# Performance work log

Measured on AMD Instinct MI355X. Metric: run time of the kernel, lower is better.

Reference implementation:

```python
import jax, jax.numpy as jnp
import numpy as np

# ---- constants derived from init kwargs (sr == down_sr => resample is identity) ----
SR = 16000
DOWN_SR = 16000
FRAME_TIME = 0.01
FMIN, FMAX = 75.0, 600.0
K = 15
TH_SIL, TH_VOI = 0.03, 0.45
C_OCT, C_JUMP, C_VUV = 0.01, 0.35, 0.14
MED = 5
STRIDES = int(DOWN_SR * FRAME_TIME)          # 160
TMAX = int(DOWN_SR // FMIN)                  # 213
TMIN = int(DOWN_SR // FMAX)                  # 26
W = int(2 ** np.ceil(np.log2(TMAX))) + 1     # 257
FLOOR = -100000.0


def setup_inputs() -> dict:
    key = jax.random.key(0)
    inputs = jax.random.normal(key, (16, 960000), dtype=jnp.float32) * 0.3
    return {"inputs": inputs}


def _nacf_forward(inputs):
    # window / normalized-autocorrelation window (buffers)
    window = 0.5 * (1.0 - jnp.cos(2.0 * jnp.pi * jnp.arange(W, dtype=jnp.float32) / W))  # periodic hann
    r = jnp.fft.rfft(window, 2 * W)
    ws = jnp.fft.irfft(r * jnp.conj(r), 2 * W)[:W]
    nacw = ws / ws[0]

    x = inputs  # resample(sr=16k -> 16k) is identity
    T = x.shape[-1]
    S = T // STRIDES + 1  # number of frames after right-pad by W
    xpad = jnp.pad(x, [(0, 0), (0, W)])
    fidx = jnp.arange(S)[:, None] * STRIDES + jnp.arange(W)[None, :]
    frames = xpad[:, fidx]                                      # [B, S, W]
    frames = (frames - frames.mean(-1, keepdims=True)) * window

    global_peak = jnp.abs(inputs).max(-1)                       # [B]
    local_peak = jnp.abs(frames).max(-1)                        # [B, S]
    intensity = jnp.where(local_peak > global_peak[:, None], 1.0,
                          local_peak / global_peak[:, None])

    # FFT-based autocorrelation, normalized
    fft = jnp.fft.rfft(frames, 2 * W, axis=-1)
    acf = jnp.fft.irfft(fft * jnp.conj(fft), 2 * W, axis=-1)[..., :W]
    nacf = acf / (acf[..., :1] * nacw)
    nacf = nacf[..., :TMAX + 1]                                 # [B, S, TMAX+1]

    d = jnp.diff(nacf, axis=-1)
    localmax = (d[..., :-1] >= 0) & (d[..., 1:] <= 0)
    flag = localmax & (nacf[..., 1:-1] > 0.5 * TH_VOI)

    n_, c_, p_ = nacf[..., 2:], nacf[..., 1:-1], nacf[..., :-2]
    dr = 0.5 * (n_ - p_) / (2.0 * c_ - n_ - p_)                 # parabolic interp
    a = jnp.arange(TMAX - 1, dtype=jnp.float32)
    freqs = DOWN_SR / (1.0 + jnp.maximum(dr + a, 0.0))          # [B, S, TMAX-1]

    logits = nacf[..., 1:TMAX]
    logits = jnp.where(logits <= 1.0, logits, 1.0 / logits)
    logits = logits - C_OCT * jnp.log2(FMIN / freqs)
    logits = jnp.where(flag, logits, FLOOR)

    logits, indices = jax.lax.top_k(logits, K)                  # [B, S, K]
    freqs = jnp.take_along_axis(freqs, indices, axis=-1)

    logits_uv = 2.0 - intensity / (TH_SIL / (1.0 + TH_VOI))
    logits_uv = TH_VOI + jnp.maximum(logits_uv, 0.0)            # [B, S]

    voiced = (logits > FLOOR) & (freqs < FMAX)                  # [B, S, K]
    delta = jnp.where(~voiced, logits_uv[..., None],
                      logits - C_OCT * jnp.log2(FMAX / freqs))

    vi = voiced[:, :-1, :, None]
    vj = voiced[:, 1:, None, :]
    trans = C_JUMP * jnp.abs(jnp.log2(freqs[:, :-1, :, None] / freqs[:, 1:, None, :]))
    trans = jnp.where(~vi & ~vj, 0.0, trans)
    trans = jnp.where(vi != vj, C_VUV, trans)                   # [B, S-1, K, K]

    # ---- Viterbi forward (scan over time) ----
    delta_t = jnp.moveaxis(delta, 1, 0)                         # [S, B, K]
    trans_t = jnp.moveaxis(trans, 1, 0)                         # [S-1, B, K, K]

    def fstep(value, xs):
        tr, dl = xs
        scores = value[..., :, None] - tr + dl[..., None, :]    # [B, K(prev), K(cur)]
        return scores.max(-2), scores.argmax(-2)

    value, ptrs = jax.lax.scan(fstep, delta_t[0], (trans_t, delta_t[1:]))

    # ---- backtrack (reverse scan) ----
    last = jnp.argmax(value, axis=-1)                           # [B]

    def bstep(s, ptr_t):
        s_new = jnp.take_along_axis(ptr_t, s[..., None], axis=-1)[..., 0]
        return s_new, s_new

    _, states_rev = jax.lax.scan(bstep, last, ptrs, reverse=True)  # [S-1, B]
    states = jnp.concatenate([jnp.moveaxis(states_rev, 0, 1), last[:, None]], axis=-1)  # [B, S]

    f_sel = jnp.take_along_axis(freqs, states[..., None], axis=-1)[..., 0]
    v_sel = jnp.take_along_axis(voiced, states[..., None], axis=-1)[..., 0]
    f0 = jnp.where(v_sel, f_sel, 0.0)                           # [B, S]

    wpad = MED // 2
    fpad = jnp.pad(f0, [(0, 0), (wpad, wpad)], mode='edge')
    widx = jnp.arange(f0.shape[-1])[:, None] + jnp.arange(MED)[None, :]
    f0 = jnp.median(fpad[:, widx], axis=-1)
    return f0


def reference(inputs):
    return _nacf_forward(inputs)
```

## Files before the change

### kernel.cpp

```cpp
#include <hip/hip_runtime.h>

#define NB 16
#define NT 960000
#define NS 6001
#define TOPK 15
#define NSTEPS 6000
#define CHUNK 100
#define NCHUNK 60
#define FLOORV -100000.0f

typedef __attribute__((ext_vector_type(8))) short short8;
typedef __attribute__((ext_vector_type(4))) float f32x4;
typedef __attribute__((ext_vector_type(2))) float f32x2;
typedef __attribute__((ext_vector_type(4))) unsigned int u32x4;

constexpr size_t OFF_NACW  = 0;
constexpr size_t OFF_WIN   = 256;
constexpr size_t OFF_GPEAK = 520;
constexpr size_t OFF_FREQ  = 576;
constexpr size_t PERFR     = (size_t)NB * NS * 16;
constexpr size_t OFF_LFV   = OFF_FREQ + PERFR;
constexpr size_t OFF_DELTA = OFF_LFV + PERFR;
constexpr size_t OFF_UNUSED= OFF_DELTA + PERFR;
constexpr size_t OFF_P     = OFF_UNUSED + PERFR;
constexpr size_t OFF_VENT  = OFF_P + (size_t)NB * NCHUNK * 256;
constexpr size_t OFF_VFIN  = OFF_VENT + (size_t)NB * (NCHUNK + 1) * 16;
constexpr size_t OFF_F0    = OFF_VFIN + 256;
constexpr size_t OFF_BS    = OFF_F0 + 96032;
constexpr size_t OFF_PTR   = OFF_BS + 2048;
constexpr size_t OFF_BMAP  = OFF_PTR + (size_t)NB * NSTEPS * 4;

__device__ __forceinline__ unsigned ordf(float f) {
  unsigned u = __float_as_uint(f);
  return (u & 0x80000000u) ? ~u : (u | 0x80000000u);
}

__device__ __forceinline__ float tr_of(float sa, float sb) {
  int xs = __float_as_int(sa) ^ __float_as_int(sb);
  float t = 0.35f * fabsf(sa - sb);
  t = (__float_as_int(sa) < 0) ? 0.f : t;
  return (xs < 0) ? 0.14f : t;
}

__global__ __launch_bounds__(256) void k_setup(float* __restrict__ ws) {
  __shared__ float win[257];
  __shared__ float w0sh;
  const int tid = threadIdx.x;
  for (int n = tid; n < 257; n += 256) {
    float w = 0.5f * (1.0f - cosf((6.2831855f * (float)n) / 257.0f));
    win[n] = w;
    ws[OFF_WIN + n] = w;
  }
  __syncthreads();
  float s = 0.f;
  if (tid < 216) {
    for (int n = 0; n + tid < 257; ++n) s += win[n] * win[n + tid];
  }
  if (tid == 0) w0sh = s;
  __syncthreads();
  if (tid < 216) ws[OFF_NACW + tid] = w0sh / s;
  if (tid < NB) ws[OFF_GPEAK + tid] = 0.0f;
}

__global__ __launch_bounds__(256) void k_gpeak(const float* __restrict__ x, float* __restrict__ ws) {
  const int b = blockIdx.y;
  const float4* xb = (const float4*)(x + (size_t)b * NT);
  const int n4 = NT / 4;
  float m = 0.f;
  for (int i = blockIdx.x * blockDim.x + threadIdx.x; i < n4; i += gridDim.x * blockDim.x) {
    float4 v = xb[i];
    m = fmaxf(m, fmaxf(fmaxf(fabsf(v.x), fabsf(v.y)), fmaxf(fabsf(v.z), fabsf(v.w))));
  }
  for (int off = 32; off; off >>= 1) m = fmaxf(m, __shfl_down(m, off));
  __shared__ float sm[4];
  if ((threadIdx.x & 63) == 0) sm[threadIdx.x >> 6] = m;
  __syncthreads();
  if (threadIdx.x == 0) {
    m = fmaxf(fmaxf(sm[0], sm[1]), fmaxf(sm[2], sm[3]));
    atomicMax((unsigned*)(ws + OFF_GPEAK) + b, __float_as_uint(m));
  }
}

__device__ __forceinline__ unsigned bf16rne(float f) {
  unsigned u = __float_as_uint(f);
  return (u + 0x7FFFu + ((u >> 16) & 1u)) >> 16;
}

__device__ __forceinline__ short8 bfrag(const char* p, int sh) {
  unsigned w0 = *(const unsigned*)(p);
  unsigned w1 = *(const unsigned*)(p + 4);
  unsigned w2 = *(const unsigned*)(p + 8);
  unsigned w3 = *(const unsigned*)(p + 12);
  unsigned w4 = *(const unsigned*)(p + 16);
  u32x4 o;
  o[0] = __builtin_amdgcn_alignbit(w1, w0, sh);
  o[1] = __builtin_amdgcn_alignbit(w2, w1, sh);
  o[2] = __builtin_amdgcn_alignbit(w3, w2, sh);
  o[3] = __builtin_amdgcn_alignbit(w4, w3, sh);
  return __builtin_bit_cast(short8, o);
}

__global__ __launch_bounds__(256, 4) void k_frames(const float* __restrict__ x, float* __restrict__ ws) {
  const int wv = threadIdx.x >> 6;
  const int g  = threadIdx.x & 63;
  const int s  = blockIdx.x * 4 + wv;
  const int b  = blockIdx.y;
  __shared__ __align__(16) float LA[4][1680];
  if (s >= NS) return;
  float* L = LA[wv];
  char* Lb = (char*)L;
  const size_t xb = (size_t)b * NT;
  const int c0 = 40 * s;

  float4 xv = make_float4(0.f, 0.f, 0.f, 0.f);
  if (c0 + g < NT / 4) xv = ((const float4*)(x + xb))[c0 + g];
  float x256 = 0.f;
  if (g == 0) {
    int i256 = 160 * s + 256;
    if (i256 < NT) x256 = x[xb + i256];
  }

  float ps = ((xv.x + xv.y) + (xv.z + xv.w)) + x256;
#pragma unroll
  for (int off = 32; off; off >>= 1) ps += __shfl_xor(ps, off);
  const float mean = ps / 257.0f;

  float4 w4 = ((const float4*)(ws + OFF_WIN))[g];
  float4 f4;
  f4.x = (xv.x - mean) * w4.x;
  f4.y = (xv.y - mean) * w4.y;
  f4.z = (xv.z - mean) * w4.z;
  f4.w = (xv.w - mean) * w4.w;
  float fr256 = 0.f;
  if (g == 0) fr256 = (x256 - mean) * ws[OFF_WIN + 256];
  float apk = fmaxf(fmaxf(fabsf(f4.x), fabsf(f4.y)), fmaxf(fabsf(f4.z), fabsf(f4.w)));
  if (g == 0) apk = fmaxf(apk, fabsf(fr256));
#pragma unroll
  for (int off = 32; off; off >>= 1) apk = fmaxf(apk, __shfl_xor(apk, off));

  {
    unsigned hx = bf16rne(f4.x), hy = bf16rne(f4.y), hz = bf16rne(f4.z), hw = bf16rne(f4.w);
    float lx = f4.x - __uint_as_float(hx << 16);
    float ly = f4.y - __uint_as_float(hy << 16);
    float lz = f4.z - __uint_as_float(hz << 16);
    float lw = f4.w - __uint_as_float(hw << 16);
    unsigned ph0 = hx | (hy << 16), ph1 = hz | (hw << 16);
    unsigned pl0 = bf16rne(lx) | (bf16rne(ly) << 16);
    unsigned pl1 = bf16rne(lz) | (bf16rne(lw) << 16);
    if (g < 8) { L[g] = 0.f; L[288 + g] = 0.f; }
    f32x2 vh = {__uint_as_float(ph0), __uint_as_float(ph1)};
    f32x2 vl = {__uint_as_float(pl0), __uint_as_float(pl1)};
    *(f32x2*)&L[8 + 2 * g] = vh;
    *(f32x2*)&L[288 + 8 + 2 * g] = vl;
    if (g < 76) {
      f32x2 z = {0.f, 0.f};
      *(f32x2*)&L[136 + 2 * g] = z;
      *(f32x2*)&L[288 + 136 + 2 * g] = z;
    }
    if (g == 0) {
      unsigned h2 = bf16rne(fr256);
      float l2 = fr256 - __uint_as_float(h2 << 16);
      ((unsigned short*)Lb)[272] = (unsigned short)h2;
      ((unsigned short*)(Lb + 1152))[272] = (unsigned short)bf16rne(l2);
    }
  }
  __builtin_amdgcn_wave_barrier();

  const int bcol = g & 15, h = g >> 4;
  const int sh = 16 * (bcol & 1);
  const int hi4 = ((bcol & 3) >= 2) ? 4 : 0;
  const int Ab0 = 16 * h + 32 * bcol;
  const int Bb0 = 16 * h + ((2 * bcol) & ~7) + hi4;
  const char* Hb = Lb;
  const char* Ob = Lb + 1152;
  f32x4 acc = {0.f, 0.f, 0.f, 0.f};
#pragma unroll
  for (int kk = 0; kk < 10; ++kk) {
    short8 ah = __builtin_bit_cast(short8, *(const u32x4*)(Hb + Ab0 + 64 * kk));
    short8 al = __builtin_bit_cast(short8, *(const u32x4*)(Ob + Ab0 + 64 * kk));
    short8 bh = bfrag(Hb + Bb0 + 64 * kk, sh);
    short8 bl = bfrag(Ob + Bb0 + 64 * kk, sh);
    acc = __builtin_amdgcn_mfma_f32_16x16x32_bf16(ah, bh, acc, 0, 0, 0);
    acc = __builtin_amdgcn_mfma_f32_16x16x32_bf16(ah, bl, acc, 0, 0, 0);
    acc = __builtin_amdgcn_mfma_f32_16x16x32_bf16(al, bh, acc, 0, 0, 0);
  }
  __builtin_amdgcn_wave_barrier();
#pragma unroll
  for (int r = 0; r < 4; ++r) {
    int arow = 4 * h + r;
    int tau = 16 * arow - bcol;
    if (arow == 0 ? (bcol == 0) : (tau <= 215)) L[576 + (arow ? tau : 0)] = acc[r];
  }
  __builtin_amdgcn_wave_barrier();

  const float inv0 = 1.0f / L[576];
  bool  flv[4] = {false, false, false, false};
  float lgv[4];
  if (g < 53) {
    f32x4 A4 = *(const f32x4*)&L[576 + 4 * g];
    f32x2 A2 = *(const f32x2*)&L[580 + 4 * g];
    f32x4 I4 = *(const f32x4*)(ws + OFF_NACW + 4 * g);
    f32x2 I2 = *(const f32x2*)(ws + OFF_NACW + 4 * g + 4);
    float nn[6];
    nn[0] = A4[0] * inv0 * I4[0];
    nn[1] = A4[1] * inv0 * I4[1];
    nn[2] = A4[2] * inv0 * I4[2];
    nn[3] = A4[3] * inv0 * I4[3];
    nn[4] = A2.x * inv0 * I2.x;
    nn[5] = A2.y * inv0 * I2.y;
    float fqv[4];
#pragma unroll
    for (int a = 0; a < 4; ++a) {
      float pm = nn[a], cm = nn[a + 1], nm = nn[a + 2];
      bool flag = (cm - pm >= 0.f) && (nm - cm <= 0.f) && (cm > 0.225f);
      float dr = (0.5f * (nm - pm)) / ((2.0f * cm - nm) - pm);
      float tq = dr + (float)(4 * g + a);
      tq = (tq > 0.f) ? tq : 0.f;
      float fq = 16000.0f / (1.0f + tq);
      float l1p = __log2f(1.0f + tq);
      float lg = cm;
      if (lg > 1.0f) lg = __builtin_amdgcn_rcpf(lg);
      lg = lg - 0.01f * (l1p - 7.736965594166206f);
      flv[a] = flag;
      fqv[a] = fq;
      lgv[a] = flag ? lg : FLOORV;
    }
    f32x4 fo = {fqv[0], fqv[1], fqv[2], fqv[3]};
    f32x4 lo_ = {lgv[0], lgv[1], lgv[2], lgv[3]};
    *(f32x4*)&L[800 + 4 * g] = fo;
    *(f32x4*)&L[1016 + 4 * g] = lo_;
  }

  unsigned long long bb0b = __ballot(flv[0]);
  unsigned long long bb1 = __ballot(flv[1]);
  unsigned long long bb2 = __ballot(flv[2]);
  unsigned long long bb3 = __ballot(flv[3]);
  const int nv = __popcll(bb0b) + __popcll(bb1) + __popcll(bb2) + __popcll(bb3);
  int* sel = (int*)&L[1656];
  if (nv > 0) {
    unsigned long long below = (1ull << g) - 1ull;
    int base = __popcll(bb0b & below) + __popcll(bb1 & below) +
               __popcll(bb2 & below) + __popcll(bb3 & below);
    if (nv <= TOPK) {
      if (g < 53) {
        int cnt = base;
#pragma unroll
        for (int a = 0; a < 4; ++a) {
          int c = 4 * g + a;
          if (flv[a]) {
            sel[cnt] = c;
            ++cnt;
          } else {
            int ur = c - cnt;
            if (ur < TOPK - nv) sel[nv + ur] = c;
          }
        }
      }
    } else {
      unsigned long long* CK = (unsigned long long*)&L[1232];
      if (g < 53) {
        int cnt = base;
#pragma unroll
        for (int a = 0; a < 4; ++a) {
          if (flv[a]) {
            CK[cnt] = (((unsigned long long)ordf(lgv[a])) << 32)
                    | (unsigned long long)(0xFFFFFFFFu - (unsigned)(4 * g + a));
            ++cnt;
          }
        }
      }
      __builtin_amdgcn_wave_barrier();
      for (int l = g; l < nv; l += 64) {
        unsigned long long kl = CK[l];
        int rank = 0;
        for (int m = 0; m < nv; ++m) rank += (CK[m] > kl) ? 1 : 0;
        if (rank < TOPK) sel[rank] = (int)(0xFFFFFFFFu - (unsigned)(kl & 0xFFFFFFFFull));
      }
    }
  }
  __builtin_amdgcn_wave_barrier();

  if (g < 16) {
    size_t fi = ((size_t)b * NS + s) * 16 + g;
    if (g == TOPK) {
      ws[OFF_FREQ + fi] = 0.f;
      ws[OFF_LFV + fi] = -1.0f;
      ws[OFF_DELTA + fi] = 0.f;
    } else {
      int c = (nv == 0) ? g : sel[g];
      float fq = L[800 + c];
      float lg = L[1016 + c];
      int voi = (lg > FLOORV) && (fq < 600.0f);
      float gp = ws[OFF_GPEAK + b];
      float inten = (apk > gp) ? 1.0f : apk * __builtin_amdgcn_rcpf(gp);
      float luv = 0.45f + fmaxf(2.0f - inten * 48.333333333333336f, 0.f);
      float l2 = __log2f(fq);
      float dlt = voi ? (lg - 0.01f * (9.228818690495881f - l2)) : luv;
      ws[OFF_FREQ + fi] = fq;
      ws[OFF_LFV + fi] = voi ? l2 : -l2;
      ws[OFF_DELTA + fi] = dlt;
    }
  }
}

__global__ __launch_bounds__(256) void k_chunkmat(float* __restrict__ ws) {
  const int c = blockIdx.x, b = blockIdx.y, tid = threadIdx.x;
  const int i = tid >> 4, j = tid & 15;
  __shared__ float Msh[16][17];
  __shared__ float Psh[2][16][17];
  const float* LFV = ws + OFF_LFV;
  const float* DEL = ws + OFF_DELTA;
  const size_t fb = (size_t)b * NS;
  const int t0 = c * CHUNK;
  float sA = LFV[(fb + t0) * 16 + i];
  float sB = LFV[(fb + t0 + 1) * 16 + j];
  float dB = DEL[(fb + t0 + 1) * 16 + j];
  Psh[0][i][j] = (i == j) ? 0.f : -INFINITY;
  int src = 0;
  float pn = 0.f;
  for (int s = 1; s <= CHUNK; ++s) {
    Msh[i][j] = dB - tr_of(sA, sB);
    __syncthreads();
    if (s < CHUNK) {
      const int t = t0 + s;
      sA = LFV[(fb + t) * 16 + i];
      sB = LFV[(fb + t + 1) * 16 + j];
      dB = DEL[(fb + t + 1) * 16 + j];
    }
    pn = -INFINITY;
#pragma unroll
    for (int k = 0; k < 15; ++k) pn = fmaxf(pn, Psh[src][i][k] + Msh[k][j]);
    Psh[src ^ 1][i][j] = pn;
    __syncthreads();
    src ^= 1;
  }
  ws[OFF_P + ((size_t)(b * NCHUNK + c)) * 256 + tid] = pn;
}

__global__ __launch_bounds__(64) void k_scan(float* __restrict__ ws) {
  const int b = blockIdx.x, l = threadIdx.x;
  __shared__ float v[16];
  const float* DEL = ws + OFF_DELTA;
  const size_t fb = (size_t)b * NS;
  if (l < 16) {
    float d0 = DEL[fb * 16 + l];
    v[l] = d0;
    ws[OFF_VENT + ((size_t)b * (NCHUNK + 1)) * 16 + l] = d0;
  }
  __syncthreads();
  const float4* Pg = (const float4*)(ws + OFF_P + (size_t)b * NCHUNK * 256);
  const int k = l >> 2;
  float4 cur = Pg[l];
  for (int c = 0; c < NCHUNK; ++c) {
    float4 nxt = cur;
    if (c + 1 < NCHUNK) nxt = Pg[(size_t)(c + 1) * 64 + l];
    float vk = (k < 15) ? v[k] : -INFINITY;
    float4 t;
    t.x = vk + cur.x; t.y = vk + cur.y; t.z = vk + cur.z; t.w = vk + cur.w;
    if (k == 15) { t.x = -INFINITY; t.y = -INFINITY; t.z = -INFINITY; t.w = -INFINITY; }
#pragma unroll
    for (int off = 4; off < 64; off <<= 1) {
      t.x = fmaxf(t.x, __shfl_xor(t.x, off));
      t.y = fmaxf(t.y, __shfl_xor(t.y, off));
      t.z = fmaxf(t.z, __shfl_xor(t.z, off));
      t.w = fmaxf(t.w, __shfl_xor(t.w, off));
    }
    __syncthreads();
    if (l < 4) {
      *(float4*)&v[4 * l] = *(float4*)&t;
      ((float4*)(ws + OFF_VENT + ((size_t)b * (NCHUNK + 1) + c + 1) * 16))[l] = *(float4*)&t;
    }
    __syncthreads();
    cur = nxt;
  }
}

__global__ __launch_bounds__(256) void k_viterbi(float* __restrict__ ws) {
  const int c = blockIdx.x, b = blockIdx.y, tid = threadIdx.x;
  const int i = tid & 15, j = tid >> 4;
  __shared__ float val[2][16];
  __shared__ __align__(16) unsigned char ptl[CHUNK][16];
  const float* LFV = ws + OFF_LFV;
  const float* DEL = ws + OFF_DELTA;
  const size_t fb = (size_t)b * NS;
  const int t0 = c * CHUNK;
  if (tid < 16) {
    val[0][tid] = ws[OFF_VENT + ((size_t)b * (NCHUNK + 1) + c) * 16 + tid];
    val[1][tid] = -INFINITY;
  }
  float sA = LFV[(fb + t0) * 16 + i];
  float sB = LFV[(fb + t0 + 1) * 16 + j];
  float dB = DEL[(fb + t0 + 1) * 16 + j];
  int src = 0;
  for (int s = 1; s <= CHUNK; ++s) {
    __syncthreads();
    float sc = (val[src][i] - tr_of(sA, sB)) + dB;
    if (i == 15) sc = -INFINITY;
    if (s < CHUNK) {
      const int t = t0 + s;
      sA = LFV[(fb + t) * 16 + i];
      sB = LFV[(fb + t + 1) * 16 + j];
      dB = DEL[(fb + t + 1) * 16 + j];
    }
    float mx = sc;
#pragma unroll
    for (int off = 1; off < 16; off <<= 1) mx = fmaxf(mx, __shfl_xor(mx, off));
    unsigned long long bal = __ballot(sc == mx);
    int nib = (int)((bal >> (tid & 48)) & 0xFFFFull);
    int bi = __ffs(nib) - 1;
    __syncthreads();
    if (i == 0 && j < 15) {
      val[src ^ 1][j] = mx;
      ptl[s - 1][j] = (unsigned char)bi;
    }
    src ^= 1;
  }
  __syncthreads();
  unsigned* pg = (unsigned*)(ws + OFF_PTR);
  for (int idx = tid; idx < CHUNK * 4; idx += 256)
    pg[((size_t)b * NSTEPS + t0) * 4 + idx] = ((unsigned*)ptl)[idx];
  if (tid < TOPK) {
    int st = tid;
#pragma unroll 1
    for (int s2 = CHUNK - 1; s2 >= 0; --s2) st = ptl[s2][st];
    ((unsigned char*)(ws + OFF_BMAP))[((size_t)(b * NCHUNK + c)) * 16 + tid] = (unsigned char)st;
  }
}

__global__ __launch_bounds__(256) void k_compose(float* __restrict__ ws) {
  __shared__ unsigned char bm[NB * NCHUNK * 16];
  const int tid = threadIdx.x;
  const unsigned char* bg = (const unsigned char*)(ws + OFF_BMAP);
  for (int idx = tid; idx < NB * NCHUNK * 16; idx += 256) bm[idx] = bg[idx];
  __syncthreads();
  if (tid < NB) {
    const int b = tid;
    float best = -INFINITY; int bi = 0;
    for (int jj = 0; jj < TOPK; ++jj) {
      float vv = ws[OFF_VENT + ((size_t)b * (NCHUNK + 1) + NCHUNK) * 16 + jj];
      if (vv > best) { best = vv; bi = jj; }
    }
    int* bs = (int*)(ws + OFF_BS);
    int st = bi;
    bs[b * (NCHUNK + 1) + NCHUNK] = st;
    for (int cc = NCHUNK - 1; cc >= 0; --cc) {
      st = bm[((size_t)(b * NCHUNK + cc)) * 16 + st];
      bs[b * (NCHUNK + 1) + cc] = st;
    }
  }
}

__global__ __launch_bounds__(64) void k_select(float* __restrict__ ws) {
  const int c = blockIdx.x, b = blockIdx.y, tid = threadIdx.x;
  __shared__ unsigned char pl[CHUNK * 16];
  __shared__ int stt[CHUNK + 1];
  const int t0 = c * CHUNK;
  const unsigned char* pg = (const unsigned char*)(ws + OFF_PTR);
  for (int idx = tid; idx < CHUNK * 16; idx += 64)
    pl[idx] = pg[((size_t)b * NSTEPS + t0) * 16 + idx];
  __syncthreads();
  if (tid == 0) {
    const int* bs = (const int*)(ws + OFF_BS);
    int st = bs[b * (NCHUNK + 1) + (c + 1)];
    stt[CHUNK] = st;
    for (int s2 = CHUNK; s2 >= 1; --s2) { st = pl[(s2 - 1) * 16 + st]; stt[s2 - 1] = st; }
  }
  __syncthreads();
  const int nt = (c == NCHUNK - 1) ? (CHUNK + 1) : CHUNK;
  for (int u = tid; u < nt; u += 64) {
    const int t = t0 + u;
    const int st = stt[u];
    size_t fi = ((size_t)b * NS + t) * 16 + st;
    float fq = ws[OFF_FREQ + fi];
    float lv = ws[OFF_LFV + fi];
    ws[OFF_F0 + (size_t)b * NS + t] = (lv > 0.f) ? fq : 0.f;
  }
}

__global__ __launch_bounds__(256) void k_median(const float* __restrict__ ws, float* __restrict__ out) {
  const int b = blockIdx.y;
  const int t = blockIdx.x * 256 + threadIdx.x;
  if (t >= NS) return;
  const float* f0 = ws + OFF_F0 + (size_t)b * NS;
  float a0 = f0[max(t - 2, 0)];
  float a1 = f0[max(t - 1, 0)];
  float a2 = f0[t];
  float a3 = f0[min(t + 1, NS - 1)];
  float a4 = f0[min(t + 2, NS - 1)];
#define SW(u, w) { float lo_ = fminf(u, w), hi_ = fmaxf(u, w); u = lo_; w = hi_; }
  SW(a0, a1) SW(a1, a2) SW(a2, a3) SW(a3, a4)
  SW(a0, a1) SW(a1, a2) SW(a2, a3)
  SW(a0, a1) SW(a1, a2)
#undef SW
  out[(size_t)b * NS + t] = a2;
}

extern "C" void kernel_launch(void* const* d_in, const int* in_sizes, int n_in,
                              void* d_out, int out_size, void* d_ws, size_t ws_size,
                              hipStream_t stream) {
  const float* x = (const float*)d_in[0];
  float* ws = (float*)d_ws;
  float* out = (float*)d_out;
  hipLaunchKernelGGL(k_setup, dim3(1), dim3(256), 0, stream, ws);
  hipLaunchKernelGGL(k_gpeak, dim3(64, NB), dim3(256), 0, stream, x, ws);
  hipLaunchKernelGGL(k_frames, dim3((NS + 3) / 4, NB), dim3(256), 0, stream, x, ws);
  hipLaunchKernelGGL(k_chunkmat, dim3(NCHUNK, NB), dim3(256), 0, stream, ws);
  hipLaunchKernelGGL(k_scan, dim3(NB), dim3(64), 0, stream, ws);
  hipLaunchKernelGGL(k_viterbi, dim3(NCHUNK, NB), dim3(256), 0, stream, ws);
  hipLaunchKernelGGL(k_compose, dim3(1), dim3(256), 0, stream, ws);
  hipLaunchKernelGGL(k_select, dim3(NCHUNK, NB), dim3(64), 0, stream, ws);
  hipLaunchKernelGGL(k_median, dim3((NS + 255) / 256, NB), dim3(256), 0, stream, ws, out);
}
```

Before: 283.4 us.

## Double-buffer chunk matrices, vectorize max-plus loads, drop barriers, defer frequency division

The chunk max-plus kernel now stores the transition matrix transposed and double-buffered with padded rows. The inner max-plus product uses 16-wide vector LDS loads, which lets one of the two barriers per step go. The Viterbi chunk kernel also loses its second barrier per step, since its value buffer is already double-buffered. In the frame kernel the frequency division moves to the 15 selected candidates only, and the occupancy hint rises from 4 to 6 blocks per CU. The risk is LDS races if the double-buffer reasoning is wrong, plus register pressure from the higher occupancy hint.

Measured after the change: 261.1 us. 1.09x faster.

```diff
diff --git a/kernel.cpp b/kernel.cpp
--- a/kernel.cpp
+++ b/kernel.cpp
@@ -100,7 +100,7 @@
   return __builtin_bit_cast(short8, o);
 }
 
-__global__ __launch_bounds__(256, 4) void k_frames(const float* __restrict__ x, float* __restrict__ ws) {
+__global__ __launch_bounds__(256, 6) void k_frames(const float* __restrict__ x, float* __restrict__ ws) {
   const int wv = threadIdx.x >> 6;
   const int g  = threadIdx.x & 63;
   const int s  = blockIdx.x * 4 + wv;
@@ -208,7 +208,7 @@
     nn[3] = A4[3] * inv0 * I4[3];
     nn[4] = A2.x * inv0 * I2.x;
     nn[5] = A2.y * inv0 * I2.y;
-    float fqv[4];
+    float tqv[4];
 #pragma unroll
     for (int a = 0; a < 4; ++a) {
       float pm = nn[a], cm = nn[a + 1], nm = nn[a + 2];
@@ -216,18 +216,17 @@
       float dr = (0.5f * (nm - pm)) / ((2.0f * cm - nm) - pm);
       float tq = dr + (float)(4 * g + a);
       tq = (tq > 0.f) ? tq : 0.f;
-      float fq = 16000.0f / (1.0f + tq);
       float l1p = __log2f(1.0f + tq);
       float lg = cm;
       if (lg > 1.0f) lg = __builtin_amdgcn_rcpf(lg);
       lg = lg - 0.01f * (l1p - 7.736965594166206f);
       flv[a] = flag;
-      fqv[a] = fq;
+      tqv[a] = tq;
       lgv[a] = flag ? lg : FLOORV;
     }
-    f32x4 fo = {fqv[0], fqv[1], fqv[2], fqv[3]};
+    f32x4 to_ = {tqv[0], tqv[1], tqv[2], tqv[3]};
     f32x4 lo_ = {lgv[0], lgv[1], lgv[2], lgv[3]};
-    *(f32x4*)&L[800 + 4 * g] = fo;
+    *(f32x4*)&L[800 + 4 * g] = to_;
     *(f32x4*)&L[1016 + 4 * g] = lo_;
   }
 
@@ -288,8 +287,9 @@
       ws[OFF_DELTA + fi] = 0.f;
     } else {
       int c = (nv == 0) ? g : sel[g];
-      float fq = L[800 + c];
+      float tq = L[800 + c];
       float lg = L[1016 + c];
+      float fq = 16000.0f / (1.0f + tq);
       int voi = (lg > FLOORV) && (fq < 600.0f);
       float gp = ws[OFF_GPEAK + b];
       float inten = (apk > gp) ? 1.0f : apk * __builtin_amdgcn_rcpf(gp);
@@ -306,8 +306,8 @@
 __global__ __launch_bounds__(256) void k_chunkmat(float* __restrict__ ws) {
   const int c = blockIdx.x, b = blockIdx.y, tid = threadIdx.x;
   const int i = tid >> 4, j = tid & 15;
-  __shared__ float Msh[16][17];
-  __shared__ float Psh[2][16][17];
+  __shared__ float MT[2][16][20];
+  __shared__ float Psh[2][16][20];
   const float* LFV = ws + OFF_LFV;
   const float* DEL = ws + OFF_DELTA;
   const size_t fb = (size_t)b * NS;
@@ -319,7 +319,8 @@
   int src = 0;
   float pn = 0.f;
   for (int s = 1; s <= CHUNK; ++s) {
-    Msh[i][j] = dB - tr_of(sA, sB);
+    const int mb = s & 1;
+    MT[mb][j][i] = dB - tr_of(sA, sB);
     __syncthreads();
     if (s < CHUNK) {
       const int t = t0 + s;
@@ -327,11 +328,18 @@
       sB = LFV[(fb + t + 1) * 16 + j];
       dB = DEL[(fb + t + 1) * 16 + j];
     }
-    pn = -INFINITY;
-#pragma unroll
-    for (int k = 0; k < 15; ++k) pn = fmaxf(pn, Psh[src][i][k] + Msh[k][j]);
+    const float* Pr = &Psh[src][i][0];
+    const float* Mr = &MT[mb][j][0];
+    f32x4 t0v = *(const f32x4*)(Pr)      + *(const f32x4*)(Mr);
+    f32x4 t1v = *(const f32x4*)(Pr + 4)  + *(const f32x4*)(Mr + 4);
+    f32x4 t2v = *(const f32x4*)(Pr + 8)  + *(const f32x4*)(Mr + 8);
+    f32x4 t3v = *(const f32x4*)(Pr + 12) + *(const f32x4*)(Mr + 12);
+    f32x4 m01 = {fmaxf(t0v[0], t0v[1]), fmaxf(t0v[2], t0v[3]), fmaxf(t1v[0], t1v[1]), fmaxf(t1v[2], t1v[3])};
+    f32x4 m23 = {fmaxf(t2v[0], t2v[1]), fmaxf(t2v[2], t2v[3]), fmaxf(t3v[0], t3v[1]), fmaxf(t3v[2], t3v[3])};
+    pn = fmaxf(fmaxf(fmaxf(m01[0], m01[1]), fmaxf(m01[2], m01[3])),
+               fmaxf(fmaxf(m23[0], m23[1]), fmaxf(m23[2], m23[3])));
+    if (j == 15) pn = -INFINITY;
     Psh[src ^ 1][i][j] = pn;
-    __syncthreads();
     src ^= 1;
   }
   ws[OFF_P + ((size_t)(b * NCHUNK + c)) * 256 + tid] = pn;
@@ -408,7 +416,6 @@
     unsigned long long bal = __ballot(sc == mx);
     int nib = (int)((bal >> (tid & 48)) & 0xFFFFull);
     int bi = __ffs(nib) - 1;
-    __syncthreads();
     if (i == 0 && j < 15) {
       val[src ^ 1][j] = mx;
       ptl[s - 1][j] = (unsigned char)bi;
```
